# Kernel optimization log

Hardware: AMD Instinct MI355X
Metric: run time of the kernel (lower is better)

Reference implementation:

```python
import jax, jax.numpy as jnp
import numpy as np

MD = 4          # search_range -> (2*MD+1)^2 = 81 correlation channels
DISP = 192      # disp_range   -> 192 horizontal displacement channels
NEG_SLOPE = 0.1


def bilinear_warp(x, flow):
    """Warp x [B,C,H,W] by pixel-offset flow [B,2,H,W] (x-offset=ch0, y-offset=ch1),
    bilinear, zeros outside (matches tf.grid_sample padding_mode='zeros')."""
    B, C, H, W = x.shape
    yy, xx = jnp.meshgrid(jnp.arange(H, dtype=x.dtype), jnp.arange(W, dtype=x.dtype), indexing='ij')
    gx = xx[None] + flow[:, 0]  # [B,H,W]
    gy = yy[None] + flow[:, 1]
    x0 = jnp.floor(gx); y0 = jnp.floor(gy)
    wx = gx - x0; wy = gy - y0
    x0i = x0.astype(jnp.int32); y0i = y0.astype(jnp.int32)

    def gather(img, xi, yi):  # img [C,H,W], xi/yi [H,W]
        valid = (xi >= 0) & (xi < W) & (yi >= 0) & (yi < H)
        xc = jnp.clip(xi, 0, W - 1); yc = jnp.clip(yi, 0, H - 1)
        return img[:, yc, xc] * valid[None].astype(img.dtype)

    def warp_one(img, x0i, y0i, wx, wy):
        v00 = gather(img, x0i,     y0i)
        v01 = gather(img, x0i + 1, y0i)
        v10 = gather(img, x0i,     y0i + 1)
        v11 = gather(img, x0i + 1, y0i + 1)
        return (v00 * (1 - wx) * (1 - wy) + v01 * wx * (1 - wy)
                + v10 * (1 - wx) * wy + v11 * wx * wy)

    return jax.vmap(warp_one)(x, x0i, y0i, wx, wy)


def corr_volume(a, b, md=MD):
    """FlowNet-style cost volume: sum over channels of a * shifted(b), zero-padded.
    a,b: [B,C,H,W] -> [B,(2md+1)^2,H,W]."""
    B, C, H, W = a.shape
    bp = jnp.pad(b, ((0, 0), (0, 0), (md, md), (md, md)))
    offs = jnp.stack(jnp.meshgrid(jnp.arange(2 * md + 1), jnp.arange(2 * md + 1),
                                  indexing='ij'), -1).reshape(-1, 2)

    def one(off):
        shifted = jax.lax.dynamic_slice(bp, (0, 0, off[0], off[1]), (B, C, H, W))
        return jnp.sum(a * shifted, axis=1)  # [B,H,W]

    return jnp.transpose(jax.vmap(one)(offs), (1, 0, 2, 3))


def disp_corr_volume(a, b, disp=DISP):
    """SpatialCorrelationSampler patch_size=(1,disp): horizontal-only cost volume,
    offsets dx in [-disp//2, disp//2 - 1]. -> [B,disp,H,W]."""
    B, C, H, W = a.shape
    half = disp // 2
    bp = jnp.pad(b, ((0, 0), (0, 0), (0, 0), (half, disp - 1 - half)))

    def one(dx):
        shifted = jax.lax.dynamic_slice(bp, (0, 0, 0, dx), (B, C, H, W))
        return jnp.sum(a * shifted, axis=1)

    return jnp.transpose(jax.vmap(one)(jnp.arange(disp)), (1, 0, 2, 3))


def lrelu(x):
    return jnp.where(x >= 0, x, NEG_SLOPE * x)


def setup_inputs() -> dict:
    key = jax.random.key(0)
    k1, k2, k3, k4 = jax.random.split(key, 4)
    B, C, H, W = 4, 64, 128, 416
    return {
        'x1': jax.random.normal(k1, (B, C, H, W), jnp.float32),
        'x2': jax.random.normal(k2, (B, C, H, W), jnp.float32),
        'r1': jax.random.normal(k3, (B, C, H, W), jnp.float32),
        'flow': jax.random.normal(k4, (B, 2, H, W), jnp.float32) * 2.0,
    }


def reference(x1, x2, r1, flow):
    x2_warp = bilinear_warp(x2, flow)                 # warping-layer grid sample
    out_corr_f = lrelu(corr_volume(x1, x2_warp))      # [B,81,H,W]
    disp_corr1 = lrelu(disp_corr_volume(x1, r1))      # [B,192,H,W]
    return jnp.concatenate([out_corr_f, disp_corr1], axis=1)  # [B,273,H,W]
```

## Files before the change

### kernel.cpp

```cpp
#include <hip/hip_runtime.h>

#define Wd 416
#define Hd 128
#define Cd 64
#define HWd 53248

typedef __attribute__((ext_vector_type(8))) short short8;
typedef __attribute__((ext_vector_type(4))) float f32x4;

__device__ __forceinline__ float bf2f(unsigned short u) {
    unsigned int v = ((unsigned int)u) << 16;
    return __builtin_bit_cast(float, v);
}
__device__ __forceinline__ unsigned short f2bf(float f) {
    unsigned int u = __builtin_bit_cast(unsigned int, f);
    u += 0x7fffu + ((u >> 16) & 1u);
    return (unsigned short)(u >> 16);
}
__device__ __forceinline__ unsigned int pk2(float lo, float hi) {
    return (unsigned int)f2bf(lo) | ((unsigned int)f2bf(hi) << 16);
}

__global__ __launch_bounds__(256) void warp_k(const float* __restrict__ x2,
                                              const float* __restrict__ flow,
                                              unsigned short* __restrict__ x2wT) {
    int gid = blockIdx.x * 256 + threadIdx.x;
    int j = gid & 7;
    int p = gid >> 3;
    int x = p % Wd;
    int t = p / Wd;
    int y = t & 127;
    int b = t >> 7;

    int fbase = ((b * 2) * Hd + y) * Wd + x;
    float fx = flow[fbase];
    float fy = flow[fbase + HWd];
    float gx = (float)x + fx;
    float gy = (float)y + fy;
    float fx0 = floorf(gx), fy0 = floorf(gy);
    float wx = gx - fx0, wy = gy - fy0;
    int x0 = (int)fx0, y0 = (int)fy0;
    bool vx0 = (unsigned)x0 < (unsigned)Wd, vx1 = (unsigned)(x0 + 1) < (unsigned)Wd;
    bool vy0 = (unsigned)y0 < (unsigned)Hd, vy1 = (unsigned)(y0 + 1) < (unsigned)Hd;
    int cx0 = min(max(x0, 0), Wd - 1), cx1 = min(max(x0 + 1, 0), Wd - 1);
    int cy0 = min(max(y0, 0), Hd - 1), cy1 = min(max(y0 + 1, 0), Hd - 1);
    float w00 = (1.f - wx) * (1.f - wy) * ((vx0 && vy0) ? 1.f : 0.f);
    float w01 = wx * (1.f - wy) * ((vx1 && vy0) ? 1.f : 0.f);
    float w10 = (1.f - wx) * wy * ((vx0 && vy1) ? 1.f : 0.f);
    float w11 = wx * wy * ((vx1 && vy1) ? 1.f : 0.f);
    int o00 = cy0 * Wd + cx0, o01 = cy0 * Wd + cx1;
    int o10 = cy1 * Wd + cx0, o11 = cy1 * Wd + cx1;

    const float* base = x2 + (long)(b * Cd + j * 8) * HWd;
    unsigned int res[4];
#pragma unroll
    for (int cc = 0; cc < 8; cc++) {
        const float* pc = base + cc * HWd;
        float v = w00 * pc[o00] + w01 * pc[o01] + w10 * pc[o10] + w11 * pc[o11];
        unsigned short h = f2bf(v);
        if (cc & 1) res[cc >> 1] |= ((unsigned int)h) << 16;
        else        res[cc >> 1] = h;
    }
    *(uint4*)(x2wT + ((long)p * Cd + j * 8)) = make_uint4(res[0], res[1], res[2], res[3]);
}

__global__ __launch_bounds__(512) void disp_k(const float* __restrict__ x1,
                                              const float* __restrict__ r1,
                                              float* __restrict__ out) {
    __shared__ unsigned short As[416 * 72];
    __shared__ unsigned short Bs[416 * 72];
    __shared__ unsigned short Ds[32 * 420];

    int tid = threadIdx.x;
    int lane = tid & 63;
    int wv = tid >> 6;
    int m = lane & 15;
    int q = lane >> 4;

    int bid = blockIdx.x;
    int b = bid >> 7;
    int y = bid & 127;

    const float* Arow = x1 + ((long)(b * Cd) * Hd + y) * Wd;
    const float* Brow = r1 + ((long)(b * Cd) * Hd + y) * Wd;

    for (int idx = tid; idx < 8 * Wd; idx += 512) {
        int x = idx % Wd;
        int oc = idx / Wd;
        const float* pa = Arow + (long)(oc * 8) * HWd + x;
        const float* pb = Brow + (long)(oc * 8) * HWd + x;
        unsigned int wa[4], wb[4];
#pragma unroll
        for (int e = 0; e < 4; e++) {
            wa[e] = pk2(pa[(2 * e) * HWd], pa[(2 * e + 1) * HWd]);
            wb[e] = pk2(pb[(2 * e) * HWd], pb[(2 * e + 1) * HWd]);
        }
        *(uint4*)&As[x * 72 + oc * 8] = make_uint4(wa[0], wa[1], wa[2], wa[3]);
        *(uint4*)&Bs[x * 72 + oc * 8] = make_uint4(wb[0], wb[1], wb[2], wb[3]);
    }

    for (int k = 0; k < 6; k++) {
        for (int idx = tid; idx < 32 * 210; idx += 512) ((unsigned int*)Ds)[idx] = 0;
        __syncthreads();

        for (int i = wv; i < 26; i += 8) {
            const unsigned short* ap = &As[(16 * i + m) * 72];
            short8 a0 = *(const short8*)(ap + q * 8);
            short8 a1 = *(const short8*)(ap + 32 + q * 8);
#pragma unroll
            for (int gg = 0; gg < 3; gg++) {
                int g = 2 * k - 6 + gg;
                int jj = i + g;
                if ((unsigned)jj >= 26u) continue;
                const unsigned short* bp = &Bs[(16 * jj + m) * 72];
                short8 b0 = *(const short8*)(bp + q * 8);
                short8 b1 = *(const short8*)(bp + 32 + q * 8);
                f32x4 acc = {0.f, 0.f, 0.f, 0.f};
                acc = __builtin_amdgcn_mfma_f32_16x16x32_bf16(a0, b0, acc, 0, 0, 0);
                acc = __builtin_amdgcn_mfma_f32_16x16x32_bf16(a1, b1, acc, 0, 0, 0);
                int dbase = 16 * g + m - 4 * q + 96 - 32 * k;
                int xb = 16 * i + 4 * q;
#pragma unroll
                for (int r = 0; r < 4; r++) {
                    int dr = dbase - r;
                    if ((unsigned)dr < 32u) {
                        float v = acc[r];
                        v = (v >= 0.f) ? v : 0.1f * v;
                        Ds[dr * 420 + xb + r] = f2bf(v);
                    }
                }
            }
        }
        __syncthreads();

        int chbase = ((b * 273 + 81 + 32 * k) * Hd + y) * Wd;
        for (int idx = tid; idx < 32 * 208; idx += 512) {
            int dr = idx / 208, xw = (idx % 208) * 2;
            *(float2*)(out + chbase + dr * HWd + xw) =
                make_float2(bf2f(Ds[dr * 420 + xw]), bf2f(Ds[dr * 420 + xw + 1]));
        }
        __syncthreads();
    }
}

__global__ __launch_bounds__(512) void corr_k(const float* __restrict__ x1,
                                              const unsigned short* __restrict__ x2wT,
                                              float* __restrict__ out) {
    __shared__ unsigned short As[2 * 208 * 72];
    __shared__ unsigned short Bs[224 * 72];
    __shared__ unsigned short Cs[9 * 212];

    int tid = threadIdx.x;
    int lane = tid & 63;
    int wv = tid >> 6;
    int m = lane & 15;
    int q = lane >> 4;

    int bid = blockIdx.x;
    int b = bid & 3;
    int y2 = (bid >> 2) & 63;
    int xh = bid >> 8;
    int y0 = y2 * 2;
    int xbase = xh * 208;

    for (int idx = tid; idx < 2 * 8 * 208; idx += 512) {
        int x = idx % 208;
        int t = idx / 208;
        int oc = t & 7, yy = t >> 3;
        const float* p = x1 + ((long)(b * Cd + oc * 8) * Hd + (y0 + yy)) * Wd + xbase + x;
        unsigned int w[4];
#pragma unroll
        for (int e = 0; e < 4; e++)
            w[e] = pk2(p[(2 * e) * HWd], p[(2 * e + 1) * HWd]);
        *(uint4*)&As[(yy * 208 + x) * 72 + oc * 8] = make_uint4(w[0], w[1], w[2], w[3]);
    }

    for (int yp = 0; yp < 10; yp++) {
        int yg = y0 - 4 + yp;
        bool yok = (unsigned)yg < (unsigned)Hd;
        __syncthreads();
        for (int idx = tid; idx < 224 * 8; idx += 512) {
            int pl = idx >> 3, co = (idx & 7) * 8;
            int xg = xbase - 4 + pl;
            uint4 v = make_uint4(0, 0, 0, 0);
            if (yok && (unsigned)xg < (unsigned)Wd)
                v = *(const uint4*)(x2wT + (((long)(b * Hd + yg) * Wd + xg) * Cd + co));
            *(uint4*)&Bs[pl * 72 + co] = v;
        }
        __syncthreads();

        for (int yy = 0; yy < 2; yy++) {
            int dy = yp - 4 - yy;
            if (dy < -4 || dy > 4) continue;

            for (int it = wv; it < 13; it += 8) {
                const unsigned short* ap = &As[(yy * 208 + 16 * it + m) * 72];
                short8 a0 = *(const short8*)(ap + q * 8);
                short8 a1 = *(const short8*)(ap + 32 + q * 8);
#pragma unroll
                for (int dj = 0; dj < 2; dj++) {
                    int jt = it + dj;
                    const unsigned short* bp = &Bs[(16 * jt + m) * 72];
                    short8 b0 = *(const short8*)(bp + q * 8);
                    short8 b1 = *(const short8*)(bp + 32 + q * 8);
                    f32x4 acc = {0.f, 0.f, 0.f, 0.f};
                    acc = __builtin_amdgcn_mfma_f32_16x16x32_bf16(a0, b0, acc, 0, 0, 0);
                    acc = __builtin_amdgcn_mfma_f32_16x16x32_bf16(a1, b1, acc, 0, 0, 0);
                    int dbase = 16 * dj + m - 4 * q;
                    int xlb = 16 * it + 4 * q;
#pragma unroll
                    for (int r = 0; r < 4; r++) {
                        int dx4 = dbase - r;
                        if ((unsigned)dx4 <= 8u) {
                            float v = acc[r];
                            v = (v >= 0.f) ? v : 0.1f * v;
                            Cs[dx4 * 212 + xlb + r] = f2bf(v);
                        }
                    }
                }
            }
            __syncthreads();

            int ch = (dy + 4) * 9;
            for (int idx = tid; idx < 9 * 104; idx += 512) {
                int orow = idx / 104, xw = (idx % 104) * 2;
                int off = ((b * 273 + ch + orow) * Hd + (y0 + yy)) * Wd + xbase + xw;
                *(float2*)(out + off) =
                    make_float2(bf2f(Cs[orow * 212 + xw]), bf2f(Cs[orow * 212 + xw + 1]));
            }
            __syncthreads();
        }
    }
}

extern "C" void kernel_launch(void* const* d_in, const int* in_sizes, int n_in,
                              void* d_out, int out_size, void* d_ws, size_t ws_size,
                              hipStream_t stream) {
    const float* x1 = (const float*)d_in[0];
    const float* x2 = (const float*)d_in[1];
    const float* r1 = (const float*)d_in[2];
    const float* fl = (const float*)d_in[3];
    float* out = (float*)d_out;
    unsigned short* x2wT = (unsigned short*)d_ws;

    warp_k<<<6656, 256, 0, stream>>>(x2, fl, x2wT);
    disp_k<<<512, 512, 0, stream>>>(x1, r1, out);
    corr_k<<<512, 512, 0, stream>>>(x1, x2wT, out);
}
```

Baseline: 533.5 us.

## Use register-resident A fragments, per-wave LDS staging and double-buffered B tiles

Both MFMA kernels now load the A operand directly from global memory into registers as bf16 fragments, so the shared A tile goes away. Results are staged in small per-wave LDS buffers guarded by wave-level fences instead of block-wide __syncthreads. B tiles use an XOR-swizzled 64-wide layout to avoid bank conflicts, and corr_k double-buffers its B rows so the next row loads while the current one computes. Together these lower LDS use, raising occupancy (launch_bounds 512,4), and remove most block barriers. The cost is more registers and strided uncoalesced global reads for the A fragments.

Measured after the change: 480.0 us. 1.11x faster.

```diff
diff --git a/kernel.cpp b/kernel.cpp
--- a/kernel.cpp
+++ b/kernel.cpp
@@ -8,6 +8,8 @@
 typedef __attribute__((ext_vector_type(8))) short short8;
 typedef __attribute__((ext_vector_type(4))) float f32x4;
 
+union frag8 { short8 s; unsigned int u[4]; };
+
 __device__ __forceinline__ float bf2f(unsigned short u) {
     unsigned int v = ((unsigned int)u) << 16;
     return __builtin_bit_cast(float, v);
@@ -19,6 +21,12 @@
 }
 __device__ __forceinline__ unsigned int pk2(float lo, float hi) {
     return (unsigned int)f2bf(lo) | ((unsigned int)f2bf(hi) << 16);
+}
+__device__ __forceinline__ float lrelu(float v) { return (v >= 0.f) ? v : 0.1f * v; }
+
+__device__ __forceinline__ void wave_fence() {
+    asm volatile("s_waitcnt lgkmcnt(0)" ::: "memory");
+    __builtin_amdgcn_sched_barrier(0);
 }
 
 __global__ __launch_bounds__(256) void warp_k(const float* __restrict__ x2,
@@ -64,12 +72,11 @@
     *(uint4*)(x2wT + ((long)p * Cd + j * 8)) = make_uint4(res[0], res[1], res[2], res[3]);
 }
 
-__global__ __launch_bounds__(512) void disp_k(const float* __restrict__ x1,
-                                              const float* __restrict__ r1,
-                                              float* __restrict__ out) {
-    __shared__ unsigned short As[416 * 72];
-    __shared__ unsigned short Bs[416 * 72];
-    __shared__ unsigned short Ds[32 * 420];
+__global__ __launch_bounds__(512, 4) void disp_k(const float* __restrict__ x1,
+                                                 const float* __restrict__ r1,
+                                                 float* __restrict__ out) {
+    __shared__ unsigned short Bs[Wd * 64];
+    __shared__ unsigned short Ds[8][96 * 16];
 
     int tid = threadIdx.x;
     int lane = tid & 63;
@@ -87,68 +94,81 @@
     for (int idx = tid; idx < 8 * Wd; idx += 512) {
         int x = idx % Wd;
         int oc = idx / Wd;
-        const float* pa = Arow + (long)(oc * 8) * HWd + x;
         const float* pb = Brow + (long)(oc * 8) * HWd + x;
-        unsigned int wa[4], wb[4];
-#pragma unroll
-        for (int e = 0; e < 4; e++) {
-            wa[e] = pk2(pa[(2 * e) * HWd], pa[(2 * e + 1) * HWd]);
+        unsigned int wb[4];
+#pragma unroll
+        for (int e = 0; e < 4; e++)
             wb[e] = pk2(pb[(2 * e) * HWd], pb[(2 * e + 1) * HWd]);
-        }
-        *(uint4*)&As[x * 72 + oc * 8] = make_uint4(wa[0], wa[1], wa[2], wa[3]);
-        *(uint4*)&Bs[x * 72 + oc * 8] = make_uint4(wb[0], wb[1], wb[2], wb[3]);
-    }
-
-    for (int k = 0; k < 6; k++) {
-        for (int idx = tid; idx < 32 * 210; idx += 512) ((unsigned int*)Ds)[idx] = 0;
-        __syncthreads();
-
-        for (int i = wv; i < 26; i += 8) {
-            const unsigned short* ap = &As[(16 * i + m) * 72];
-            short8 a0 = *(const short8*)(ap + q * 8);
-            short8 a1 = *(const short8*)(ap + 32 + q * 8);
-#pragma unroll
-            for (int gg = 0; gg < 3; gg++) {
-                int g = 2 * k - 6 + gg;
+        *(uint4*)&Bs[x * 64 + ((oc ^ (x & 7)) * 8)] = make_uint4(wb[0], wb[1], wb[2], wb[3]);
+    }
+
+    frag8 a0[4], a1[4];
+#pragma unroll
+    for (int t = 0; t < 4; t++) {
+        int i = wv + 8 * t;
+        if (i < 26) {
+            const float* pa = Arow + 16 * i + m;
+#pragma unroll
+            for (int k = 0; k < 4; k++) {
+                a0[t].u[k] = pk2(pa[(8 * q + 2 * k) * HWd], pa[(8 * q + 2 * k + 1) * HWd]);
+                a1[t].u[k] = pk2(pa[(32 + 8 * q + 2 * k) * HWd], pa[(32 + 8 * q + 2 * k + 1) * HWd]);
+            }
+        }
+    }
+    __syncthreads();
+
+    unsigned short* Dw = Ds[wv];
+#pragma unroll
+    for (int h = 0; h < 2; h++) {
+#pragma unroll
+        for (int t = 0; t < 4; t++) {
+            int i = wv + 8 * t;
+            if (i >= 26) continue;
+#pragma unroll
+            for (int z = 0; z < 3; z++)
+                *(uint4*)&Dw[(lane + 64 * z) * 8] = make_uint4(0, 0, 0, 0);
+            wave_fence();
+#pragma unroll
+            for (int gg = 0; gg < 7; gg++) {
+                int g = h ? gg : gg - 6;
                 int jj = i + g;
                 if ((unsigned)jj >= 26u) continue;
-                const unsigned short* bp = &Bs[(16 * jj + m) * 72];
-                short8 b0 = *(const short8*)(bp + q * 8);
-                short8 b1 = *(const short8*)(bp + 32 + q * 8);
+                int xp = 16 * jj + m;
+                const unsigned short* bp = &Bs[xp * 64];
+                short8 b0 = *(const short8*)(bp + ((q ^ (xp & 7)) * 8));
+                short8 b1 = *(const short8*)(bp + (((q + 4) ^ (xp & 7)) * 8));
                 f32x4 acc = {0.f, 0.f, 0.f, 0.f};
-                acc = __builtin_amdgcn_mfma_f32_16x16x32_bf16(a0, b0, acc, 0, 0, 0);
-                acc = __builtin_amdgcn_mfma_f32_16x16x32_bf16(a1, b1, acc, 0, 0, 0);
-                int dbase = 16 * g + m - 4 * q + 96 - 32 * k;
-                int xb = 16 * i + 4 * q;
+                acc = __builtin_amdgcn_mfma_f32_16x16x32_bf16(a0[t].s, b0, acc, 0, 0, 0);
+                acc = __builtin_amdgcn_mfma_f32_16x16x32_bf16(a1[t].s, b1, acc, 0, 0, 0);
+                int dbase = 16 * g + m - 4 * q + 96 - 96 * h;
 #pragma unroll
                 for (int r = 0; r < 4; r++) {
-                    int dr = dbase - r;
-                    if ((unsigned)dr < 32u) {
-                        float v = acc[r];
-                        v = (v >= 0.f) ? v : 0.1f * v;
-                        Ds[dr * 420 + xb + r] = f2bf(v);
-                    }
+                    int d = dbase - r;
+                    if ((unsigned)d < 96u)
+                        Dw[d * 16 + 4 * q + r] = f2bf(lrelu(acc[r]));
                 }
             }
-        }
-        __syncthreads();
-
-        int chbase = ((b * 273 + 81 + 32 * k) * Hd + y) * Wd;
-        for (int idx = tid; idx < 32 * 208; idx += 512) {
-            int dr = idx / 208, xw = (idx % 208) * 2;
-            *(float2*)(out + chbase + dr * HWd + xw) =
-                make_float2(bf2f(Ds[dr * 420 + xw]), bf2f(Ds[dr * 420 + xw + 1]));
-        }
-        __syncthreads();
-    }
-}
-
-__global__ __launch_bounds__(512) void corr_k(const float* __restrict__ x1,
-                                              const unsigned short* __restrict__ x2wT,
-                                              float* __restrict__ out) {
-    __shared__ unsigned short As[2 * 208 * 72];
-    __shared__ unsigned short Bs[224 * 72];
-    __shared__ unsigned short Cs[9 * 212];
+            wave_fence();
+            long chb = ((long)(b * 273 + 81 + 96 * h) * Hd + y) * Wd + 16 * i;
+#pragma unroll
+            for (int k = 0; k < 12; k++) {
+                int e = 64 * k + lane;
+                unsigned int w = *(unsigned int*)&Dw[e * 2];
+                int d = e >> 3, xx = (e & 7) * 2;
+                *(float2*)(out + chb + (long)d * HWd + xx) =
+                    make_float2(bf2f((unsigned short)(w & 0xffffu)),
+                                bf2f((unsigned short)(w >> 16)));
+            }
+            wave_fence();
+        }
+    }
+}
+
+__global__ __launch_bounds__(512, 4) void corr_k(const float* __restrict__ x1,
+                                                 const unsigned short* __restrict__ x2wT,
+                                                 float* __restrict__ out) {
+    __shared__ unsigned short Bs[2][224 * 64];
+    __shared__ unsigned short Cs[8][160];
 
     int tid = threadIdx.x;
     int lane = tid & 63;
@@ -163,73 +183,82 @@
     int y0 = y2 * 2;
     int xbase = xh * 208;
 
-    for (int idx = tid; idx < 2 * 8 * 208; idx += 512) {
-        int x = idx % 208;
-        int t = idx / 208;
-        int oc = t & 7, yy = t >> 3;
-        const float* p = x1 + ((long)(b * Cd + oc * 8) * Hd + (y0 + yy)) * Wd + xbase + x;
-        unsigned int w[4];
-#pragma unroll
-        for (int e = 0; e < 4; e++)
-            w[e] = pk2(p[(2 * e) * HWd], p[(2 * e + 1) * HWd]);
-        *(uint4*)&As[(yy * 208 + x) * 72 + oc * 8] = make_uint4(w[0], w[1], w[2], w[3]);
-    }
-
-    for (int yp = 0; yp < 10; yp++) {
+    int yy = wv & 1;
+    int it0 = wv >> 1;
+
+    frag8 a0[4], a1[4];
+#pragma unroll
+    for (int t = 0; t < 4; t++) {
+        int it = it0 + 4 * t;
+        if (it < 13) {
+            const float* pa = x1 + ((long)(b * Cd) * Hd + (y0 + yy)) * Wd + xbase + 16 * it + m;
+#pragma unroll
+            for (int k = 0; k < 4; k++) {
+                a0[t].u[k] = pk2(pa[(8 * q + 2 * k) * HWd], pa[(8 * q + 2 * k + 1) * HWd]);
+                a1[t].u[k] = pk2(pa[(32 + 8 * q + 2 * k) * HWd], pa[(32 + 8 * q + 2 * k + 1) * HWd]);
+            }
+        }
+    }
+
+    auto stage = [&](int yp, int sel) {
         int yg = y0 - 4 + yp;
         bool yok = (unsigned)yg < (unsigned)Hd;
-        __syncthreads();
         for (int idx = tid; idx < 224 * 8; idx += 512) {
-            int pl = idx >> 3, co = (idx & 7) * 8;
+            int pl = idx >> 3, oc = idx & 7;
             int xg = xbase - 4 + pl;
             uint4 v = make_uint4(0, 0, 0, 0);
             if (yok && (unsigned)xg < (unsigned)Wd)
-                v = *(const uint4*)(x2wT + (((long)(b * Hd + yg) * Wd + xg) * Cd + co));
-            *(uint4*)&Bs[pl * 72 + co] = v;
-        }
-        __syncthreads();
-
-        for (int yy = 0; yy < 2; yy++) {
-            int dy = yp - 4 - yy;
-            if (dy < -4 || dy > 4) continue;
-
-            for (int it = wv; it < 13; it += 8) {
-                const unsigned short* ap = &As[(yy * 208 + 16 * it + m) * 72];
-                short8 a0 = *(const short8*)(ap + q * 8);
-                short8 a1 = *(const short8*)(ap + 32 + q * 8);
+                v = *(const uint4*)(x2wT + (((long)(b * Hd + yg) * Wd + xg) * Cd + oc * 8));
+            *(uint4*)&Bs[sel][pl * 64 + ((oc ^ (pl & 7)) * 8)] = v;
+        }
+    };
+
+    stage(0, 0);
+    __syncthreads();
+
+    for (int yp = 0; yp < 10; yp++) {
+        int cur = yp & 1;
+        if (yp < 9) stage(yp + 1, cur ^ 1);
+        int dy = yp - 4 - yy;
+        if ((unsigned)(dy + 4) <= 8u) {
+            long obase = ((long)(b * 273 + (dy + 4) * 9) * Hd + (y0 + yy)) * Wd + xbase;
+#pragma unroll
+            for (int t = 0; t < 4; t++) {
+                int it = it0 + 4 * t;
+                if (it >= 13) continue;
 #pragma unroll
                 for (int dj = 0; dj < 2; dj++) {
-                    int jt = it + dj;
-                    const unsigned short* bp = &Bs[(16 * jt + m) * 72];
-                    short8 b0 = *(const short8*)(bp + q * 8);
-                    short8 b1 = *(const short8*)(bp + 32 + q * 8);
+                    int pl = 16 * (it + dj) + m;
+                    const unsigned short* bp = &Bs[cur][pl * 64];
+                    short8 b0 = *(const short8*)(bp + ((q ^ (pl & 7)) * 8));
+                    short8 b1 = *(const short8*)(bp + (((q + 4) ^ (pl & 7)) * 8));
                     f32x4 acc = {0.f, 0.f, 0.f, 0.f};
-                    acc = __builtin_amdgcn_mfma_f32_16x16x32_bf16(a0, b0, acc, 0, 0, 0);
-                    acc = __builtin_amdgcn_mfma_f32_16x16x32_bf16(a1, b1, acc, 0, 0, 0);
+                    acc = __builtin_amdgcn_mfma_f32_16x16x32_bf16(a0[t].s, b0, acc, 0, 0, 0);
+                    acc = __builtin_amdgcn_mfma_f32_16x16x32_bf16(a1[t].s, b1, acc, 0, 0, 0);
                     int dbase = 16 * dj + m - 4 * q;
-                    int xlb = 16 * it + 4 * q;
 #pragma unroll
                     for (int r = 0; r < 4; r++) {
                         int dx4 = dbase - r;
-                        if ((unsigned)dx4 <= 8u) {
-                            float v = acc[r];
-                            v = (v >= 0.f) ? v : 0.1f * v;
-                            Cs[dx4 * 212 + xlb + r] = f2bf(v);
-                        }
+                        if ((unsigned)dx4 <= 8u)
+                            Cs[wv][dx4 * 16 + 4 * q + r] = f2bf(lrelu(acc[r]));
                     }
                 }
-            }
-            __syncthreads();
-
-            int ch = (dy + 4) * 9;
-            for (int idx = tid; idx < 9 * 104; idx += 512) {
-                int orow = idx / 104, xw = (idx % 104) * 2;
-                int off = ((b * 273 + ch + orow) * Hd + (y0 + yy)) * Wd + xbase + xw;
-                *(float2*)(out + off) =
-                    make_float2(bf2f(Cs[orow * 212 + xw]), bf2f(Cs[orow * 212 + xw + 1]));
-            }
-            __syncthreads();
-        }
+                wave_fence();
+#pragma unroll
+                for (int k = 0; k < 2; k++) {
+                    int e = 64 * k + lane;
+                    if (e < 72) {
+                        unsigned int w = *(unsigned int*)&Cs[wv][e * 2];
+                        int dxr = e >> 3, xx = (e & 7) * 2;
+                        *(float2*)(out + obase + (long)dxr * HWd + 16 * it + xx) =
+                            make_float2(bf2f((unsigned short)(w & 0xffffu)),
+                                        bf2f((unsigned short)(w >> 16)));
+                    }
+                }
+                wave_fence();
+            }
+        }
+        __syncthreads();
     }
 }
 
```
